# Kernel tuning notes

Hardware: AMD Instinct MI355X
Metric: run time of the kernel (lower is better)

Reference implementation:

```python
import jax, jax.numpy as jnp
from jax import lax
import numpy as np

B, T, IN, H = 1024, 512, 16, 64


def _gru_layer(x_seq, W_ih, W_hh, b_ih, b_hh):
    """PyTorch-convention GRU layer. x_seq: [B,T,in] -> (outputs [B,T,H], h_last [B,H])."""
    # Precompute input contributions for all timesteps: [B,T,3H]
    gx_all = jnp.einsum('bti,gi->btg', x_seq, W_ih) + b_ih

    def step(h, gx):
        gh = h @ W_hh.T + b_hh                      # [B,3H]
        xr, xz, xn = jnp.split(gx, 3, axis=-1)
        hr, hz, hn = jnp.split(gh, 3, axis=-1)
        r = jax.nn.sigmoid(xr + hr)
        z = jax.nn.sigmoid(xz + hz)
        n = jnp.tanh(xn + r * hn)
        h_new = (1.0 - z) * n + z * h
        return h_new, h_new

    h0 = jnp.zeros((x_seq.shape[0], W_hh.shape[1]), x_seq.dtype)
    h_last, hs = lax.scan(step, h0, jnp.swapaxes(gx_all, 0, 1))  # hs: [T,B,H]
    return jnp.swapaxes(hs, 0, 1), h_last


def setup_inputs() -> dict:
    key = jax.random.key(0)
    ks = jax.random.split(key, 16)
    s = 0.1  # init scale ~ 1/sqrt(H)
    inp = {
        'x': jax.random.normal(ks[0], (B, T, IN), jnp.float32),
        'W_ih0': jax.random.normal(ks[1], (3 * H, IN), jnp.float32) * s,
        'W_hh0': jax.random.normal(ks[2], (3 * H, H), jnp.float32) * s,
        'b_ih0': jax.random.normal(ks[3], (3 * H,), jnp.float32) * s,
        'b_hh0': jax.random.normal(ks[4], (3 * H,), jnp.float32) * s,
        'W_ih1': jax.random.normal(ks[5], (3 * H, H), jnp.float32) * s,
        'W_hh1': jax.random.normal(ks[6], (3 * H, H), jnp.float32) * s,
        'b_ih1': jax.random.normal(ks[7], (3 * H,), jnp.float32) * s,
        'b_hh1': jax.random.normal(ks[8], (3 * H,), jnp.float32) * s,
        'W_ih2': jax.random.normal(ks[9], (3 * H, H), jnp.float32) * s,
        'W_hh2': jax.random.normal(ks[10], (3 * H, H), jnp.float32) * s,
        'b_ih2': jax.random.normal(ks[11], (3 * H,), jnp.float32) * s,
        'b_hh2': jax.random.normal(ks[12], (3 * H,), jnp.float32) * s,
        'fc1_w': jax.random.normal(ks[13], (32, H), jnp.float32) * s,
        'fc1_b': jnp.zeros((32,), jnp.float32),
        'fc2_w': jax.random.normal(ks[14], (1, 32), jnp.float32) * s,
        'fc2_b': jnp.zeros((1,), jnp.float32),
    }
    return inp


def reference(x, W_ih0, W_hh0, b_ih0, b_hh0,
              W_ih1, W_hh1, b_ih1, b_hh1,
              W_ih2, W_hh2, b_ih2, b_hh2,
              fc1_w, fc1_b, fc2_w, fc2_b):
    # 3-layer GRU (dropout is identity in eval mode)
    out0, _ = _gru_layer(x, W_ih0, W_hh0, b_ih0, b_hh0)
    out1, _ = _gru_layer(out0, W_ih1, W_hh1, b_ih1, b_hh1)
    _, h_last = _gru_layer(out1, W_ih2, W_hh2, b_ih2, b_hh2)  # h[-1]: [B,H]
    z = jax.nn.relu(h_last @ fc1_w.T + fc1_b)                 # [B,32]
    y = z @ fc2_w.T + fc2_b                                   # [B,1]
    return y
```

## Files before the change

### kernel.cpp

```cpp
#include <hip/hip_runtime.h>

#define TT 512

typedef __attribute__((ext_vector_type(8))) short bf16x8;
typedef __attribute__((ext_vector_type(4))) short s16x4;
typedef __attribute__((ext_vector_type(4))) float f32x4;

__device__ inline short f2bf(float f) {
    unsigned u = __float_as_uint(f);
    u += 0x7FFFu + ((u >> 16) & 1u);
    return (short)(u >> 16);
}

__device__ inline float sigm(float x)  { return __fdividef(1.0f, 1.0f + __expf(-x)); }
__device__ inline float tanh_(float x) { return 1.0f - __fdividef(2.0f, 1.0f + __expf(2.0f * x)); }

#define MFMA16(a, b, c) __builtin_amdgcn_mfma_f32_16x16x32_bf16((a), (b), (c), 0, 0, 0)

__global__ __launch_bounds__(768, 1)
void gru_fused(const float* __restrict__ x,
               const float* __restrict__ Wih0, const float* __restrict__ Whh0,
               const float* __restrict__ bih0, const float* __restrict__ bhh0,
               const float* __restrict__ Wih1, const float* __restrict__ Whh1,
               const float* __restrict__ bih1, const float* __restrict__ bhh1,
               const float* __restrict__ Wih2, const float* __restrict__ Whh2,
               const float* __restrict__ bih2, const float* __restrict__ bhh2,
               const float* __restrict__ fc1w, const float* __restrict__ fc1b,
               const float* __restrict__ fc2w, const float* __restrict__ fc2b,
               float* __restrict__ out)
{
    __shared__ __align__(16) short xls[TT][4][32];
    __shared__ __align__(16) short hbuf[3][2][4 * 80];
    __shared__ float h2out[4][64];
    __shared__ float fcz[4][32];

    const int tid = threadIdx.x;
    const int l   = tid & 63;
    const int wid = tid >> 6;
    const int Ls  = __builtin_amdgcn_readfirstlane(wid >> 2);
    const int qt  = wid & 3;
    const int n_  = l & 15;
    const int q   = l >> 4;
    const int ar  = n_ >> 2;
    const int rbase = blockIdx.x * 4;
    const int grow = q;
    const int u    = qt * 16 + n_;

    for (int i = tid; i < 3 * 2 * 320; i += 768) (&hbuf[0][0][0])[i] = 0;
    {
        const f32x4 z4 = {0.f, 0.f, 0.f, 0.f};
        for (int i = tid; i < 4096; i += 768) {
            const int t = i >> 3, sub = i & 7;
            *(f32x4*)&xls[t][sub >> 1][16 + (sub & 1) * 8] = z4;
        }
    }

    {
        const float4* xv = (const float4*)(x + (size_t)rbase * (TT * 16));
        auto stash = [&](int i, float4 v) {
            const int row = i >> 11, rem = i & 2047;
            s16x4 pv = { f2bf(v.x), f2bf(v.y), f2bf(v.z), f2bf(v.w) };
            *(s16x4*)&xls[rem >> 2][row][(rem & 3) * 4] = pv;
        };
        for (int base = tid; base < 8192; base += 3072) {
            const int i1 = base + 768, i2 = base + 1536, i3 = base + 2304;
            float4 v0 = xv[base], v1, v2, v3;
            if (i1 < 8192) v1 = xv[i1];
            if (i2 < 8192) v2 = xv[i2];
            if (i3 < 8192) v3 = xv[i3];
            stash(base, v0);
            if (i1 < 8192) stash(i1, v1);
            if (i2 < 8192) stash(i2, v2);
            if (i3 < 8192) stash(i3, v3);
        }
    }

    const float* Wih = (Ls == 0) ? Wih0 : (Ls == 1) ? Wih1 : Wih2;
    const float* Whh = (Ls == 0) ? Whh0 : (Ls == 1) ? Whh1 : Whh2;
    const float* bih = (Ls == 0) ? bih0 : (Ls == 1) ? bih1 : bih2;
    const float* bhh = (Ls == 0) ? bhh0 : (Ls == 1) ? bhh1 : bhh2;
    const int ldih = (Ls == 0) ? 16 : 64;

    bf16x8 wihf[3][2], whhf[3][2];
#pragma unroll
    for (int g = 0; g < 3; ++g) {
        const int gc = g * 64 + qt * 16;
#pragma unroll
        for (int kt = 0; kt < 2; ++kt) {
            const int kb = kt * 32 + q * 8;
            bf16x8 fi, fh;
#pragma unroll
            for (int j = 0; j < 8; ++j) {
                const int k = kb + j;
                float vi = (k < ldih) ? Wih[(gc + n_) * ldih + k] : 0.0f;
                float vh = Whh[(gc + n_) * 64 + k];
                fi[j] = f2bf(vi);
                fh[j] = f2bf(vh);
            }
            wihf[g][kt] = fi;
            whhf[g][kt] = fh;
        }
    }

    const float br  = bih[u] + bhh[u];
    const float bz  = bih[64 + u] + bhh[64 + u];
    const float bxn = bih[128 + u];
    const float bhn = bhh[128 + u];
    const f32x4 fbr  = {br,  br,  br,  br};
    const f32x4 fbz  = {bz,  bz,  bz,  bz};
    const f32x4 fbxn = {bxn, bxn, bxn, bxn};
    const f32x4 fbhn = {bhn, bhn, bhn, bhn};

    float hp = 0.0f;
    __syncthreads();

#define GRU_STEP(sv, par)                                                        \
    {                                                                            \
        const int tw = (sv) - Ls;                                                \
        if (tw >= 0 && tw < TT) {                                                \
            const int bi = (par) ^ (Ls & 1);                                     \
            const short* own = &hbuf[Ls][bi ^ 1][0];                             \
            const bf16x8 hA0 = *(const bf16x8*)(own + ar * 80 + q * 8);          \
            const bf16x8 hA1 = *(const bf16x8*)(own + ar * 80 + 32 + q * 8);     \
            f32x4 cr, cz, cxn;                                                   \
            if (Ls == 0) {                                                       \
                const bf16x8 iA0 = *(const bf16x8*)(&xls[tw][0][0] + ar * 32 + q * 8); \
                cr  = MFMA16(iA0, wihf[0][0], fbr);                              \
                cz  = MFMA16(iA0, wihf[1][0], fbz);                              \
                cxn = MFMA16(iA0, wihf[2][0], fbxn);                             \
            } else {                                                             \
                const short* inp = &hbuf[Ls - 1][bi][0];                         \
                const bf16x8 iA0 = *(const bf16x8*)(inp + ar * 80 + q * 8);      \
                const bf16x8 iA1 = *(const bf16x8*)(inp + ar * 80 + 32 + q * 8); \
                cr  = MFMA16(iA0, wihf[0][0], fbr);                              \
                cr  = MFMA16(iA1, wihf[0][1], cr);                               \
                cz  = MFMA16(iA0, wihf[1][0], fbz);                              \
                cz  = MFMA16(iA1, wihf[1][1], cz);                               \
                cxn = MFMA16(iA0, wihf[2][0], fbxn);                             \
                cxn = MFMA16(iA1, wihf[2][1], cxn);                              \
            }                                                                    \
            cr  = MFMA16(hA0, whhf[0][0], cr);                                   \
            cr  = MFMA16(hA1, whhf[0][1], cr);                                   \
            cz  = MFMA16(hA0, whhf[1][0], cz);                                   \
            cz  = MFMA16(hA1, whhf[1][1], cz);                                   \
            f32x4 chn = MFMA16(hA0, whhf[2][0], fbhn);                           \
            chn = MFMA16(hA1, whhf[2][1], chn);                                  \
            const float rr = sigm(cr[0]);                                        \
            const float zz = sigm(cz[0]);                                        \
            const float nn = tanh_(cxn[0] + rr * chn[0]);                        \
            const float hv = nn + zz * (hp - nn);                                \
            hp = hv;                                                             \
            hbuf[Ls][bi][grow * 80 + u] = f2bf(hv);                              \
        }                                                                        \
        __syncthreads();                                                         \
    }

    for (int s0 = 0; s0 < TT + 2; s0 += 2) {
        GRU_STEP(s0, 0)
        GRU_STEP(s0 + 1, 1)
    }
#undef GRU_STEP

    if (wid >= 8) h2out[grow][u] = hp;
    __syncthreads();
    if (tid < 128) {
        const int row = tid >> 5, uu = tid & 31;
        float acc = fc1b[uu];
#pragma unroll
        for (int k = 0; k < 64; ++k) acc += h2out[row][k] * fc1w[uu * 64 + k];
        fcz[row][uu] = fmaxf(acc, 0.0f);
    }
    __syncthreads();
    if (tid < 4) {
        float y = fc2b[0];
#pragma unroll
        for (int uu = 0; uu < 32; ++uu) y += fcz[tid][uu] * fc2w[uu];
        out[rbase + tid] = y;
    }
}

extern "C" void kernel_launch(void* const* d_in, const int* in_sizes, int n_in,
                              void* d_out, int out_size, void* d_ws, size_t ws_size,
                              hipStream_t stream) {
    (void)in_sizes; (void)n_in; (void)d_ws; (void)ws_size; (void)out_size;
    gru_fused<<<dim3(256), dim3(768), 0, stream>>>(
        (const float*)d_in[0],
        (const float*)d_in[1],  (const float*)d_in[2],  (const float*)d_in[3],  (const float*)d_in[4],
        (const float*)d_in[5],  (const float*)d_in[6],  (const float*)d_in[7],  (const float*)d_in[8],
        (const float*)d_in[9],  (const float*)d_in[10], (const float*)d_in[11], (const float*)d_in[12],
        (const float*)d_in[13], (const float*)d_in[14], (const float*)d_in[15], (const float*)d_in[16],
        (float*)d_out);
}
```

Baseline: 407.4 us.

## Replace per-step block barriers with LDS counter-based producer/consumer sync across layers

Drops the lockstep __syncthreads wavefront schedule, where every layer advanced one step per barrier. Each layer's four waves now publish per-wave step counters in LDS and spin on them, and hidden states pass through an 8-deep ring buffer so layers can run ahead of each other and decouple. This removes the block-wide barrier cost per timestep and lets layer pipelines overlap with slack. In exchange it adds spin-polling with sleep, volatile counter reads and fence overhead, and it relies on LDS memory ordering being correct. The x staging is also shrunk to 16 columns, with the zero-padding now done through predicated register loads.

Result: slower. 480.4 us (+17.9%).

```diff
diff --git a/kernel.cpp b/kernel.cpp
--- a/kernel.cpp
+++ b/kernel.cpp
@@ -29,8 +29,9 @@
                const float* __restrict__ fc2w, const float* __restrict__ fc2b,
                float* __restrict__ out)
 {
-    __shared__ __align__(16) short xls[TT][4][32];
-    __shared__ __align__(16) short hbuf[3][2][4 * 80];
+    __shared__ __align__(16) short xls[TT][4][16];
+    __shared__ __align__(16) short hring[3][8][4 * 80];
+    __shared__ __align__(8) unsigned short cnt[3][4];
     __shared__ float h2out[4][64];
     __shared__ float fcz[4][32];
 
@@ -46,32 +47,16 @@
     const int grow = q;
     const int u    = qt * 16 + n_;
 
-    for (int i = tid; i < 3 * 2 * 320; i += 768) (&hbuf[0][0][0])[i] = 0;
-    {
-        const f32x4 z4 = {0.f, 0.f, 0.f, 0.f};
-        for (int i = tid; i < 4096; i += 768) {
-            const int t = i >> 3, sub = i & 7;
-            *(f32x4*)&xls[t][sub >> 1][16 + (sub & 1) * 8] = z4;
-        }
-    }
+    for (int i = tid; i < 3 * 8 * 320; i += 768) (&hring[0][0][0])[i] = 0;
+    if (tid < 12) (&cnt[0][0])[tid] = 0;
 
     {
         const float4* xv = (const float4*)(x + (size_t)rbase * (TT * 16));
-        auto stash = [&](int i, float4 v) {
+        for (int i = tid; i < 8192; i += 768) {
+            float4 v = xv[i];
             const int row = i >> 11, rem = i & 2047;
             s16x4 pv = { f2bf(v.x), f2bf(v.y), f2bf(v.z), f2bf(v.w) };
             *(s16x4*)&xls[rem >> 2][row][(rem & 3) * 4] = pv;
-        };
-        for (int base = tid; base < 8192; base += 3072) {
-            const int i1 = base + 768, i2 = base + 1536, i3 = base + 2304;
-            float4 v0 = xv[base], v1, v2, v3;
-            if (i1 < 8192) v1 = xv[i1];
-            if (i2 < 8192) v2 = xv[i2];
-            if (i3 < 8192) v3 = xv[i3];
-            stash(base, v0);
-            if (i1 < 8192) stash(i1, v1);
-            if (i2 < 8192) stash(i2, v2);
-            if (i3 < 8192) stash(i3, v3);
         }
     }
 
@@ -111,55 +96,70 @@
     const f32x4 fbxn = {bxn, bxn, bxn, bxn};
     const f32x4 fbhn = {bhn, bhn, bhn, bhn};
 
+    auto rd4min = [&](int LL) -> int {
+        unsigned long long v = *(volatile const unsigned long long*)&cnt[LL][0];
+        unsigned a = (unsigned)(v & 0xFFFFu), b = (unsigned)((v >> 16) & 0xFFFFu);
+        unsigned c = (unsigned)((v >> 32) & 0xFFFFu), d = (unsigned)(v >> 48);
+        unsigned m0 = a < b ? a : b, m1 = c < d ? c : d;
+        return (int)(m0 < m1 ? m0 : m1);
+    };
+
     float hp = 0.0f;
     __syncthreads();
 
-#define GRU_STEP(sv, par)                                                        \
-    {                                                                            \
-        const int tw = (sv) - Ls;                                                \
-        if (tw >= 0 && tw < TT) {                                                \
-            const int bi = (par) ^ (Ls & 1);                                     \
-            const short* own = &hbuf[Ls][bi ^ 1][0];                             \
-            const bf16x8 hA0 = *(const bf16x8*)(own + ar * 80 + q * 8);          \
-            const bf16x8 hA1 = *(const bf16x8*)(own + ar * 80 + 32 + q * 8);     \
-            f32x4 cr, cz, cxn;                                                   \
-            if (Ls == 0) {                                                       \
-                const bf16x8 iA0 = *(const bf16x8*)(&xls[tw][0][0] + ar * 32 + q * 8); \
-                cr  = MFMA16(iA0, wihf[0][0], fbr);                              \
-                cz  = MFMA16(iA0, wihf[1][0], fbz);                              \
-                cxn = MFMA16(iA0, wihf[2][0], fbxn);                             \
-            } else {                                                             \
-                const short* inp = &hbuf[Ls - 1][bi][0];                         \
-                const bf16x8 iA0 = *(const bf16x8*)(inp + ar * 80 + q * 8);      \
-                const bf16x8 iA1 = *(const bf16x8*)(inp + ar * 80 + 32 + q * 8); \
-                cr  = MFMA16(iA0, wihf[0][0], fbr);                              \
-                cr  = MFMA16(iA1, wihf[0][1], cr);                               \
-                cz  = MFMA16(iA0, wihf[1][0], fbz);                              \
-                cz  = MFMA16(iA1, wihf[1][1], cz);                               \
-                cxn = MFMA16(iA0, wihf[2][0], fbxn);                             \
-                cxn = MFMA16(iA1, wihf[2][1], cxn);                              \
-            }                                                                    \
-            cr  = MFMA16(hA0, whhf[0][0], cr);                                   \
-            cr  = MFMA16(hA1, whhf[0][1], cr);                                   \
-            cz  = MFMA16(hA0, whhf[1][0], cz);                                   \
-            cz  = MFMA16(hA1, whhf[1][1], cz);                                   \
-            f32x4 chn = MFMA16(hA0, whhf[2][0], fbhn);                           \
-            chn = MFMA16(hA1, whhf[2][1], chn);                                  \
-            const float rr = sigm(cr[0]);                                        \
-            const float zz = sigm(cz[0]);                                        \
-            const float nn = tanh_(cxn[0] + rr * chn[0]);                        \
-            const float hv = nn + zz * (hp - nn);                                \
-            hp = hv;                                                             \
-            hbuf[Ls][bi][grow * 80 + u] = f2bf(hv);                              \
-        }                                                                        \
-        __syncthreads();                                                         \
+    int mc_sib = 0, mc_in = 0, mc_thr = 0;
+
+    for (int t = 0; t < TT; ++t) {
+        f32x4 cr, cz, cxn;
+        if (Ls == 0) {
+            bf16x8 iA0 = {0,0,0,0,0,0,0,0};
+            if (q < 2) iA0 = *(const bf16x8*)(&xls[t][ar][q * 8]);
+            cr  = MFMA16(iA0, wihf[0][0], fbr);
+            cz  = MFMA16(iA0, wihf[1][0], fbz);
+            cxn = MFMA16(iA0, wihf[2][0], fbxn);
+        } else {
+            while (mc_in <= t) {
+                mc_in = rd4min(Ls - 1);
+                if (mc_in <= t) __builtin_amdgcn_s_sleep(1);
+            }
+            asm volatile("" ::: "memory");
+            const short* rin = &hring[Ls - 1][t & 7][0];
+            const bf16x8 iA0 = *(const bf16x8*)(rin + ar * 80 + q * 8);
+            const bf16x8 iA1 = *(const bf16x8*)(rin + ar * 80 + 32 + q * 8);
+            cr  = MFMA16(iA0, wihf[0][0], fbr);  cr  = MFMA16(iA1, wihf[0][1], cr);
+            cz  = MFMA16(iA0, wihf[1][0], fbz);  cz  = MFMA16(iA1, wihf[1][1], cz);
+            cxn = MFMA16(iA0, wihf[2][0], fbxn); cxn = MFMA16(iA1, wihf[2][1], cxn);
+        }
+
+        while (mc_sib < t) {
+            mc_sib = rd4min(Ls);
+            if (mc_sib < t) __builtin_amdgcn_s_sleep(1);
+        }
+        asm volatile("" ::: "memory");
+        const short* own = &hring[Ls][(t - 1) & 7][0];
+        const bf16x8 hA0 = *(const bf16x8*)(own + ar * 80 + q * 8);
+        const bf16x8 hA1 = *(const bf16x8*)(own + ar * 80 + 32 + q * 8);
+        cr  = MFMA16(hA0, whhf[0][0], cr);   cr  = MFMA16(hA1, whhf[0][1], cr);
+        cz  = MFMA16(hA0, whhf[1][0], cz);   cz  = MFMA16(hA1, whhf[1][1], cz);
+        f32x4 chn = MFMA16(hA0, whhf[2][0], fbhn);
+        chn = MFMA16(hA1, whhf[2][1], chn);
+
+        const float rr = sigm(cr[0]);
+        const float zz = sigm(cz[0]);
+        const float nn = tanh_(cxn[0] + rr * chn[0]);
+        const float hv = nn + zz * (hp - nn);
+        hp = hv;
+
+        if (Ls < 2) {
+            while (mc_thr < t - 7) {
+                mc_thr = rd4min(Ls + 1);
+                if (mc_thr < t - 7) __builtin_amdgcn_s_sleep(1);
+            }
+        }
+        hring[Ls][t & 7][grow * 80 + u] = f2bf(hv);
+        __threadfence_block();
+        if (l == 0) *(volatile unsigned short*)&cnt[Ls][qt] = (unsigned short)(t + 1);
     }
-
-    for (int s0 = 0; s0 < TT + 2; s0 += 2) {
-        GRU_STEP(s0, 0)
-        GRU_STEP(s0 + 1, 1)
-    }
-#undef GRU_STEP
 
     if (wid >= 8) h2out[grow][u] = hp;
     __syncthreads();
```

## Broadcast MFMA A-fragments via DPP, prescale weights for exp2, split input/hidden chains

Applied to the files above, without the earlier changes.

Only one lane in four reads the h/x A-operand fragments from LDS, and the values go to the other lanes with DPP quad broadcasts. This cuts redundant LDS traffic on the serial recurrence path. Gate weights and biases are prescaled by -log2e or 2*log2e so the activations use exp2f directly. The input-path and hidden-path MFMA chains are split into independent accumulators to shorten the dependency chain. The x LDS buffer is shrunk by dropping padding, and layer-0 lanes q>=2 feed zeros, which adds DPP instructions and extra adds in exchange.

Measured after the change: 497.1 us. +22.0%, slower.

```diff
diff --git a/kernel.cpp b/kernel.cpp
--- a/kernel.cpp
+++ b/kernel.cpp
@@ -12,8 +12,14 @@
     return (short)(u >> 16);
 }
 
-__device__ inline float sigm(float x)  { return __fdividef(1.0f, 1.0f + __expf(-x)); }
-__device__ inline float tanh_(float x) { return 1.0f - __fdividef(2.0f, 1.0f + __expf(2.0f * x)); }
+__device__ inline bf16x8 qbcast(int4 t) {
+    int4 r;
+    r.x = __builtin_amdgcn_mov_dpp(t.x, 0, 0xF, 0xF, true);
+    r.y = __builtin_amdgcn_mov_dpp(t.y, 0, 0xF, 0xF, true);
+    r.z = __builtin_amdgcn_mov_dpp(t.z, 0, 0xF, 0xF, true);
+    r.w = __builtin_amdgcn_mov_dpp(t.w, 0, 0xF, 0xF, true);
+    union { int4 i; bf16x8 b; } u_; u_.i = r; return u_.b;
+}
 
 #define MFMA16(a, b, c) __builtin_amdgcn_mfma_f32_16x16x32_bf16((a), (b), (c), 0, 0, 0)
 
@@ -29,7 +35,7 @@
                const float* __restrict__ fc2w, const float* __restrict__ fc2b,
                float* __restrict__ out)
 {
-    __shared__ __align__(16) short xls[TT][4][32];
+    __shared__ __align__(16) short xls[TT][4][16];
     __shared__ __align__(16) short hbuf[3][2][4 * 80];
     __shared__ float h2out[4][64];
     __shared__ float fcz[4][32];
@@ -45,33 +51,17 @@
     const int rbase = blockIdx.x * 4;
     const int grow = q;
     const int u    = qt * 16 + n_;
+    const bool rd  = ((l & 3) == 0);
 
     for (int i = tid; i < 3 * 2 * 320; i += 768) (&hbuf[0][0][0])[i] = 0;
-    {
-        const f32x4 z4 = {0.f, 0.f, 0.f, 0.f};
-        for (int i = tid; i < 4096; i += 768) {
-            const int t = i >> 3, sub = i & 7;
-            *(f32x4*)&xls[t][sub >> 1][16 + (sub & 1) * 8] = z4;
-        }
-    }
 
     {
         const float4* xv = (const float4*)(x + (size_t)rbase * (TT * 16));
-        auto stash = [&](int i, float4 v) {
+        for (int i = tid; i < 8192; i += 768) {
+            float4 v = xv[i];
             const int row = i >> 11, rem = i & 2047;
             s16x4 pv = { f2bf(v.x), f2bf(v.y), f2bf(v.z), f2bf(v.w) };
             *(s16x4*)&xls[rem >> 2][row][(rem & 3) * 4] = pv;
-        };
-        for (int base = tid; base < 8192; base += 3072) {
-            const int i1 = base + 768, i2 = base + 1536, i3 = base + 2304;
-            float4 v0 = xv[base], v1, v2, v3;
-            if (i1 < 8192) v1 = xv[i1];
-            if (i2 < 8192) v2 = xv[i2];
-            if (i3 < 8192) v3 = xv[i3];
-            stash(base, v0);
-            if (i1 < 8192) stash(i1, v1);
-            if (i2 < 8192) stash(i2, v2);
-            if (i3 < 8192) stash(i3, v3);
         }
     }
 
@@ -81,10 +71,14 @@
     const float* bhh = (Ls == 0) ? bhh0 : (Ls == 1) ? bhh1 : bhh2;
     const int ldih = (Ls == 0) ? 16 : 64;
 
+    const float L2E = 1.44269504088896f;
+    const float gsc0 = -L2E, gsc1 = -L2E, gsc2 = 2.0f * L2E;
+
     bf16x8 wihf[3][2], whhf[3][2];
 #pragma unroll
     for (int g = 0; g < 3; ++g) {
         const int gc = g * 64 + qt * 16;
+        const float sc = (g == 0) ? gsc0 : (g == 1) ? gsc1 : gsc2;
 #pragma unroll
         for (int kt = 0; kt < 2; ++kt) {
             const int kb = kt * 32 + q * 8;
@@ -94,65 +88,86 @@
                 const int k = kb + j;
                 float vi = (k < ldih) ? Wih[(gc + n_) * ldih + k] : 0.0f;
                 float vh = Whh[(gc + n_) * 64 + k];
-                fi[j] = f2bf(vi);
-                fh[j] = f2bf(vh);
+                fi[j] = f2bf(vi * sc);
+                fh[j] = f2bf(vh * sc);
             }
             wihf[g][kt] = fi;
             whhf[g][kt] = fh;
         }
     }
 
-    const float br  = bih[u] + bhh[u];
-    const float bz  = bih[64 + u] + bhh[64 + u];
-    const float bxn = bih[128 + u];
-    const float bhn = bhh[128 + u];
+    const float br  = gsc0 * (bih[u] + bhh[u]);
+    const float bz  = gsc1 * (bih[64 + u] + bhh[64 + u]);
+    const float bxn = gsc2 * bih[128 + u];
+    const float bhn = gsc2 * bhh[128 + u];
     const f32x4 fbr  = {br,  br,  br,  br};
     const f32x4 fbz  = {bz,  bz,  bz,  bz};
     const f32x4 fbxn = {bxn, bxn, bxn, bxn};
     const f32x4 fbhn = {bhn, bhn, bhn, bhn};
+    const f32x4 zf4  = {0.f, 0.f, 0.f, 0.f};
+    const bf16x8 zero8 = {0,0,0,0,0,0,0,0};
+
+    int4 th0 = {0,0,0,0}, th1 = {0,0,0,0};
+    int4 ti0 = {0,0,0,0}, ti1 = {0,0,0,0};
+    int4 tx0 = {0,0,0,0};
 
     float hp = 0.0f;
     __syncthreads();
 
-#define GRU_STEP(sv, par)                                                        \
-    {                                                                            \
-        const int tw = (sv) - Ls;                                                \
-        if (tw >= 0 && tw < TT) {                                                \
-            const int bi = (par) ^ (Ls & 1);                                     \
-            const short* own = &hbuf[Ls][bi ^ 1][0];                             \
-            const bf16x8 hA0 = *(const bf16x8*)(own + ar * 80 + q * 8);          \
-            const bf16x8 hA1 = *(const bf16x8*)(own + ar * 80 + 32 + q * 8);     \
-            f32x4 cr, cz, cxn;                                                   \
-            if (Ls == 0) {                                                       \
-                const bf16x8 iA0 = *(const bf16x8*)(&xls[tw][0][0] + ar * 32 + q * 8); \
-                cr  = MFMA16(iA0, wihf[0][0], fbr);                              \
-                cz  = MFMA16(iA0, wihf[1][0], fbz);                              \
-                cxn = MFMA16(iA0, wihf[2][0], fbxn);                             \
-            } else {                                                             \
-                const short* inp = &hbuf[Ls - 1][bi][0];                         \
-                const bf16x8 iA0 = *(const bf16x8*)(inp + ar * 80 + q * 8);      \
-                const bf16x8 iA1 = *(const bf16x8*)(inp + ar * 80 + 32 + q * 8); \
-                cr  = MFMA16(iA0, wihf[0][0], fbr);                              \
-                cr  = MFMA16(iA1, wihf[0][1], cr);                               \
-                cz  = MFMA16(iA0, wihf[1][0], fbz);                              \
-                cz  = MFMA16(iA1, wihf[1][1], cz);                               \
-                cxn = MFMA16(iA0, wihf[2][0], fbxn);                             \
-                cxn = MFMA16(iA1, wihf[2][1], cxn);                              \
-            }                                                                    \
-            cr  = MFMA16(hA0, whhf[0][0], cr);                                   \
-            cr  = MFMA16(hA1, whhf[0][1], cr);                                   \
-            cz  = MFMA16(hA0, whhf[1][0], cz);                                   \
-            cz  = MFMA16(hA1, whhf[1][1], cz);                                   \
-            f32x4 chn = MFMA16(hA0, whhf[2][0], fbhn);                           \
-            chn = MFMA16(hA1, whhf[2][1], chn);                                  \
-            const float rr = sigm(cr[0]);                                        \
-            const float zz = sigm(cz[0]);                                        \
-            const float nn = tanh_(cxn[0] + rr * chn[0]);                        \
-            const float hv = nn + zz * (hp - nn);                                \
-            hp = hv;                                                             \
-            hbuf[Ls][bi][grow * 80 + u] = f2bf(hv);                              \
-        }                                                                        \
-        __syncthreads();                                                         \
+#define GRU_STEP(sv, par)                                                          \
+    {                                                                              \
+        const int tw = (sv) - Ls;                                                  \
+        if (tw >= 0 && tw < TT) {                                                  \
+            const int bi = (par) ^ (Ls & 1);                                       \
+            const short* own = &hbuf[Ls][bi ^ 1][0];                               \
+            if (rd) {                                                              \
+                th0 = *(const int4*)(own + ar * 80 + q * 8);                       \
+                th1 = *(const int4*)(own + ar * 80 + 32 + q * 8);                  \
+            }                                                                      \
+            const bf16x8 hA0 = qbcast(th0);                                        \
+            const bf16x8 hA1 = qbcast(th1);                                        \
+            f32x4 ci_r, ci_z, ci_n;                                                \
+            if (Ls == 0) {                                                         \
+                bf16x8 xA0 = zero8;                                                \
+                if (q < 2) {                                                       \
+                    if (rd) tx0 = *(const int4*)(&xls[tw][ar][q * 8]);             \
+                    xA0 = qbcast(tx0);                                             \
+                }                                                                  \
+                ci_r = MFMA16(xA0, wihf[0][0], fbr);                               \
+                ci_z = MFMA16(xA0, wihf[1][0], fbz);                               \
+                ci_n = MFMA16(xA0, wihf[2][0], fbxn);                              \
+            } else {                                                               \
+                const short* inp = &hbuf[Ls - 1][bi][0];                           \
+                if (rd) {                                                          \
+                    ti0 = *(const int4*)(inp + ar * 80 + q * 8);                   \
+                    ti1 = *(const int4*)(inp + ar * 80 + 32 + q * 8);              \
+                }                                                                  \
+                const bf16x8 iA0 = qbcast(ti0);                                    \
+                const bf16x8 iA1 = qbcast(ti1);                                    \
+                ci_r = MFMA16(iA0, wihf[0][0], fbr);                               \
+                ci_r = MFMA16(iA1, wihf[0][1], ci_r);                              \
+                ci_z = MFMA16(iA0, wihf[1][0], fbz);                               \
+                ci_z = MFMA16(iA1, wihf[1][1], ci_z);                              \
+                ci_n = MFMA16(iA0, wihf[2][0], fbxn);                              \
+                ci_n = MFMA16(iA1, wihf[2][1], ci_n);                              \
+            }                                                                      \
+            f32x4 ch_r = MFMA16(hA0, whhf[0][0], zf4);                             \
+            ch_r = MFMA16(hA1, whhf[0][1], ch_r);                                  \
+            f32x4 ch_z = MFMA16(hA0, whhf[1][0], zf4);                             \
+            ch_z = MFMA16(hA1, whhf[1][1], ch_z);                                  \
+            f32x4 ch_n = MFMA16(hA0, whhf[2][0], fbhn);                            \
+            ch_n = MFMA16(hA1, whhf[2][1], ch_n);                                  \
+            const float pr = ci_r[0] + ch_r[0];                                    \
+            const float pz = ci_z[0] + ch_z[0];                                    \
+            const float rr = __fdividef(1.0f, 1.0f + exp2f(pr));                   \
+            const float zz = __fdividef(1.0f, 1.0f + exp2f(pz));                   \
+            const float sn = ci_n[0] + rr * ch_n[0];                               \
+            const float nn = 1.0f - __fdividef(2.0f, 1.0f + exp2f(sn));            \
+            const float hv = nn + zz * (hp - nn);                                  \
+            hp = hv;                                                               \
+            hbuf[Ls][bi][grow * 80 + u] = f2bf(hv);                                \
+        }                                                                          \
+        __syncthreads();                                                           \
     }
 
     for (int s0 = 0; s0 < TT + 2; s0 += 2) {
```

## Assign one wavefront per GRU layer and fold exp2 scaling into weights

Applied to the files above, without the earlier changes.

The block shrinks from 12 wavefronts (four per layer, each owning 16 hidden units) to 3 wavefronts, one per layer, each computing all 64 hidden units with four MFMA tiles per gate. The log2(e) and 2·log2(e) factors are folded into the bf16 weights and biases so the activations use exp2f directly. Each wave reloads its own new hidden state from LDS right after writing it, which keeps the recurrent operand in registers across the barrier. The aim is to cut per-step barrier and cross-wave latency in the serial recurrence. The cost is four times as many MFMAs serialized inside each wave, and zero-padded MFMAs for the 16-wide layer-0 input.

Measured after the change: 676.6 us. 1.66x slower.

```diff
diff --git a/kernel.cpp b/kernel.cpp
--- a/kernel.cpp
+++ b/kernel.cpp
@@ -12,12 +12,9 @@
     return (short)(u >> 16);
 }
 
-__device__ inline float sigm(float x)  { return __fdividef(1.0f, 1.0f + __expf(-x)); }
-__device__ inline float tanh_(float x) { return 1.0f - __fdividef(2.0f, 1.0f + __expf(2.0f * x)); }
-
 #define MFMA16(a, b, c) __builtin_amdgcn_mfma_f32_16x16x32_bf16((a), (b), (c), 0, 0, 0)
 
-__global__ __launch_bounds__(768, 1)
+__global__ __launch_bounds__(192, 1)
 void gru_fused(const float* __restrict__ x,
                const float* __restrict__ Wih0, const float* __restrict__ Whh0,
                const float* __restrict__ bih0, const float* __restrict__ bhh0,
@@ -29,7 +26,7 @@
                const float* __restrict__ fc2w, const float* __restrict__ fc2b,
                float* __restrict__ out)
 {
-    __shared__ __align__(16) short xls[TT][4][32];
+    __shared__ __align__(16) short xls[TT][4][16];
     __shared__ __align__(16) short hbuf[3][2][4 * 80];
     __shared__ float h2out[4][64];
     __shared__ float fcz[4][32];
@@ -37,41 +34,21 @@
     const int tid = threadIdx.x;
     const int l   = tid & 63;
     const int wid = tid >> 6;
-    const int Ls  = __builtin_amdgcn_readfirstlane(wid >> 2);
-    const int qt  = wid & 3;
+    const int Ls  = __builtin_amdgcn_readfirstlane(wid);
     const int n_  = l & 15;
     const int q   = l >> 4;
     const int ar  = n_ >> 2;
     const int rbase = blockIdx.x * 4;
-    const int grow = q;
-    const int u    = qt * 16 + n_;
 
-    for (int i = tid; i < 3 * 2 * 320; i += 768) (&hbuf[0][0][0])[i] = 0;
-    {
-        const f32x4 z4 = {0.f, 0.f, 0.f, 0.f};
-        for (int i = tid; i < 4096; i += 768) {
-            const int t = i >> 3, sub = i & 7;
-            *(f32x4*)&xls[t][sub >> 1][16 + (sub & 1) * 8] = z4;
-        }
-    }
+    for (int i = tid; i < 3 * 2 * 320; i += 192) (&hbuf[0][0][0])[i] = 0;
 
     {
         const float4* xv = (const float4*)(x + (size_t)rbase * (TT * 16));
-        auto stash = [&](int i, float4 v) {
+        for (int i = tid; i < 8192; i += 192) {
+            float4 v = xv[i];
             const int row = i >> 11, rem = i & 2047;
             s16x4 pv = { f2bf(v.x), f2bf(v.y), f2bf(v.z), f2bf(v.w) };
             *(s16x4*)&xls[rem >> 2][row][(rem & 3) * 4] = pv;
-        };
-        for (int base = tid; base < 8192; base += 3072) {
-            const int i1 = base + 768, i2 = base + 1536, i3 = base + 2304;
-            float4 v0 = xv[base], v1, v2, v3;
-            if (i1 < 8192) v1 = xv[i1];
-            if (i2 < 8192) v2 = xv[i2];
-            if (i3 < 8192) v3 = xv[i3];
-            stash(base, v0);
-            if (i1 < 8192) stash(i1, v1);
-            if (i2 < 8192) stash(i2, v2);
-            if (i3 < 8192) stash(i3, v3);
         }
     }
 
@@ -81,10 +58,13 @@
     const float* bhh = (Ls == 0) ? bhh0 : (Ls == 1) ? bhh1 : bhh2;
     const int ldih = (Ls == 0) ? 16 : 64;
 
-    bf16x8 wihf[3][2], whhf[3][2];
+    const float L2E = 1.44269504088896f;
+
+    bf16x8 wihf[12][2], whhf[12][2];
 #pragma unroll
-    for (int g = 0; g < 3; ++g) {
-        const int gc = g * 64 + qt * 16;
+    for (int ti = 0; ti < 12; ++ti) {
+        const int gc = ti * 16;
+        const float sc = (ti < 8) ? -L2E : 2.0f * L2E;
 #pragma unroll
         for (int kt = 0; kt < 2; ++kt) {
             const int kb = kt * 32 + q * 8;
@@ -94,24 +74,29 @@
                 const int k = kb + j;
                 float vi = (k < ldih) ? Wih[(gc + n_) * ldih + k] : 0.0f;
                 float vh = Whh[(gc + n_) * 64 + k];
-                fi[j] = f2bf(vi);
-                fh[j] = f2bf(vh);
+                fi[j] = f2bf(vi * sc);
+                fh[j] = f2bf(vh * sc);
             }
-            wihf[g][kt] = fi;
-            whhf[g][kt] = fh;
+            wihf[ti][kt] = fi;
+            whhf[ti][kt] = fh;
         }
     }
 
-    const float br  = bih[u] + bhh[u];
-    const float bz  = bih[64 + u] + bhh[64 + u];
-    const float bxn = bih[128 + u];
-    const float bhn = bhh[128 + u];
-    const f32x4 fbr  = {br,  br,  br,  br};
-    const f32x4 fbz  = {bz,  bz,  bz,  bz};
-    const f32x4 fbxn = {bxn, bxn, bxn, bxn};
-    const f32x4 fbhn = {bhn, bhn, bhn, bhn};
+    float br_[4], bz_[4], bxn_[4], bhn_[4];
+#pragma unroll
+    for (int k = 0; k < 4; ++k) {
+        const int c = k * 16 + n_;
+        br_[k]  = -L2E * (bih[c] + bhh[c]);
+        bz_[k]  = -L2E * (bih[64 + c] + bhh[64 + c]);
+        bxn_[k] = 2.0f * L2E * bih[128 + c];
+        bhn_[k] = 2.0f * L2E * bhh[128 + c];
+    }
 
-    float hp = 0.0f;
+    const f32x4 zf4 = {0.f, 0.f, 0.f, 0.f};
+    const bf16x8 zero8 = {0,0,0,0,0,0,0,0};
+    bf16x8 hA0 = zero8, hA1 = zero8;
+    float hp[4] = {0.f, 0.f, 0.f, 0.f};
+
     __syncthreads();
 
 #define GRU_STEP(sv, par)                                                        \
@@ -119,38 +104,54 @@
         const int tw = (sv) - Ls;                                                \
         if (tw >= 0 && tw < TT) {                                                \
             const int bi = (par) ^ (Ls & 1);                                     \
-            const short* own = &hbuf[Ls][bi ^ 1][0];                             \
-            const bf16x8 hA0 = *(const bf16x8*)(own + ar * 80 + q * 8);          \
-            const bf16x8 hA1 = *(const bf16x8*)(own + ar * 80 + 32 + q * 8);     \
-            f32x4 cr, cz, cxn;                                                   \
+                   \
+            bf16x8 iA0 = zero8, iA1 = zero8;                                     \
             if (Ls == 0) {                                                       \
-                const bf16x8 iA0 = *(const bf16x8*)(&xls[tw][0][0] + ar * 32 + q * 8); \
-                cr  = MFMA16(iA0, wihf[0][0], fbr);                              \
-                cz  = MFMA16(iA0, wihf[1][0], fbz);                              \
-                cxn = MFMA16(iA0, wihf[2][0], fbxn);                             \
+                if (q < 2) iA0 = *(const bf16x8*)(&xls[tw][ar][q * 8]);          \
             } else {                                                             \
                 const short* inp = &hbuf[Ls - 1][bi][0];                         \
-                const bf16x8 iA0 = *(const bf16x8*)(inp + ar * 80 + q * 8);      \
-                const bf16x8 iA1 = *(const bf16x8*)(inp + ar * 80 + 32 + q * 8); \
-                cr  = MFMA16(iA0, wihf[0][0], fbr);                              \
-                cr  = MFMA16(iA1, wihf[0][1], cr);                               \
-                cz  = MFMA16(iA0, wihf[1][0], fbz);                              \
-                cz  = MFMA16(iA1, wihf[1][1], cz);                               \
-                cxn = MFMA16(iA0, wihf[2][0], fbxn);                             \
-                cxn = MFMA16(iA1, wihf[2][1], cxn);                              \
+                iA0 = *(const bf16x8*)(inp + ar * 80 + q * 8);                   \
+                iA1 = *(const bf16x8*)(inp + ar * 80 + 32 + q * 8);              \
             }                                                                    \
-            cr  = MFMA16(hA0, whhf[0][0], cr);                                   \
-            cr  = MFMA16(hA1, whhf[0][1], cr);                                   \
-            cz  = MFMA16(hA0, whhf[1][0], cz);                                   \
-            cz  = MFMA16(hA1, whhf[1][1], cz);                                   \
-            f32x4 chn = MFMA16(hA0, whhf[2][0], fbhn);                           \
-            chn = MFMA16(hA1, whhf[2][1], chn);                                  \
-            const float rr = sigm(cr[0]);                                        \
-            const float zz = sigm(cz[0]);                                        \
-            const float nn = tanh_(cxn[0] + rr * chn[0]);                        \
-            const float hv = nn + zz * (hp - nn);                                \
-            hp = hv;                                                             \
-            hbuf[Ls][bi][grow * 80 + u] = f2bf(hv);                              \
+                      \
+            f32x4 accr[4], accz[4], cin[4], chn_[4];                             \
+            _Pragma("unroll")                                                    \
+            for (int k = 0; k < 4; ++k) {                                        \
+                accr[k] = MFMA16(hA0, whhf[k][0], zf4);                          \
+                accr[k] = MFMA16(hA1, whhf[k][1], accr[k]);                      \
+                accz[k] = MFMA16(hA0, whhf[4 + k][0], zf4);                      \
+                accz[k] = MFMA16(hA1, whhf[4 + k][1], accz[k]);                  \
+                chn_[k] = MFMA16(hA0, whhf[8 + k][0], zf4);                      \
+                chn_[k] = MFMA16(hA1, whhf[8 + k][1], chn_[k]);                  \
+            }                                                                    \
+            _Pragma("unroll")                                                    \
+            for (int k = 0; k < 4; ++k) {                                        \
+                accr[k] = MFMA16(iA0, wihf[k][0], accr[k]);                      \
+                accr[k] = MFMA16(iA1, wihf[k][1], accr[k]);                      \
+                accz[k] = MFMA16(iA0, wihf[4 + k][0], accz[k]);                  \
+                accz[k] = MFMA16(iA1, wihf[4 + k][1], accz[k]);                  \
+                cin[k]  = MFMA16(iA0, wihf[8 + k][0], zf4);                      \
+                cin[k]  = MFMA16(iA1, wihf[8 + k][1], cin[k]);                   \
+            }                                                                    \
+                    \
+            float hv_[4];                                                        \
+            _Pragma("unroll")                                                    \
+            for (int k = 0; k < 4; ++k) {                                        \
+                const float pr = accr[k][0] + br_[k];                            \
+                const float pz = accz[k][0] + bz_[k];                            \
+                const float rr = __fdividef(1.0f, 1.0f + exp2f(pr));             \
+                const float zz = __fdividef(1.0f, 1.0f + exp2f(pz));             \
+                const float sn = (cin[k][0] + bxn_[k]) + rr * (chn_[k][0] + bhn_[k]); \
+                const float nn = 1.0f - __fdividef(2.0f, 1.0f + exp2f(sn));      \
+                const float hv = nn + zz * (hp[k] - nn);                         \
+                hp[k] = hv; hv_[k] = hv;                                         \
+            }                                                                    \
+                \
+            short* ob = &hbuf[Ls][bi][0];                                        \
+            _Pragma("unroll")                                                    \
+            for (int k = 0; k < 4; ++k) ob[q * 80 + k * 16 + n_] = f2bf(hv_[k]); \
+            hA0 = *(const bf16x8*)(ob + ar * 80 + q * 8);                        \
+            hA1 = *(const bf16x8*)(ob + ar * 80 + 32 + q * 8);                   \
         }                                                                        \
         __syncthreads();                                                         \
     }
@@ -161,7 +162,10 @@
     }
 #undef GRU_STEP
 
-    if (wid >= 8) h2out[grow][u] = hp;
+    if (wid == 2) {
+#pragma unroll
+        for (int k = 0; k < 4; ++k) h2out[q][k * 16 + n_] = hp[k];
+    }
     __syncthreads();
     if (tid < 128) {
         const int row = tid >> 5, uu = tid & 31;
@@ -183,7 +187,7 @@
                               void* d_out, int out_size, void* d_ws, size_t ws_size,
                               hipStream_t stream) {
     (void)in_sizes; (void)n_in; (void)d_ws; (void)ws_size; (void)out_size;
-    gru_fused<<<dim3(256), dim3(768), 0, stream>>>(
+    gru_fused<<<dim3(256), dim3(192), 0, stream>>>(
         (const float*)d_in[0],
         (const float*)d_in[1],  (const float*)d_in[2],  (const float*)d_in[3],  (const float*)d_in[4],
         (const float*)d_in[5],  (const float*)d_in[6],  (const float*)d_in[7],  (const float*)d_in[8],
```
